# Performance work log

Measured on AMD Instinct MI355X. Metric: run time of the kernel, lower is better.

The kernel has to match this reference:

```python
import jax, jax.numpy as jnp
import numpy as np

NBINS = (128, 64, 32)
N_POINTS = 250_000
N_GENES = 5000
N_GENES_OI = 500
SUM_H = sum(NBINS)            # 224
SUM_W = sum(n - 1 for n in NBINS)  # 221


def _calculate_widths(unnormalized_widths):
    return jax.nn.softmax(unnormalized_widths, axis=-1)


def _calculate_bin_locations(widths):
    bl = jnp.cumsum(widths, axis=-1)
    bl = bl.at[..., -1].set(1.0)
    pad = [(0, 0)] * (bl.ndim - 1) + [(1, 0)]
    return jnp.pad(bl, pad)


def _calculate_heights(unnormalized_heights, widths):
    e = jnp.exp(unnormalized_heights)
    # trapezoid-rule area so pdf integrates to 1
    area = jnp.sum(0.5 * (e[..., :-1] + e[..., 1:]) * widths, axis=-1, keepdims=True)
    return e / area


def _calculate_bin_left_cdf(heights, widths):
    cdf = jnp.cumsum(0.5 * (heights[..., :-1] + heights[..., 1:]) * widths, axis=-1)
    cdf = cdf.at[..., -1].set(1.0)
    pad = [(0, 0)] * (cdf.ndim - 1) + [(1, 0)]
    return jnp.pad(cdf, pad)


def _quadratic_spline(x, widths, heights, bin_left_cdf, bin_locations):
    # all per-point: widths [N,nb], heights [N,nb+1], cdf/locations [N,nb+1]
    nb = widths.shape[-1]
    bin_idx = jnp.clip(jnp.sum(x[:, None] >= bin_locations, axis=-1) - 1, 0, nb - 1)

    def take(a, i):
        return jnp.take_along_axis(a, i[:, None], axis=-1)[:, 0]

    in_bl = take(bin_locations, bin_idx)
    in_cdf = take(bin_left_cdf, bin_idx)
    h_left = take(heights, bin_idx)
    h_right = take(heights, bin_idx + 1)
    w = take(widths, bin_idx)

    a = 0.5 * (h_right - h_left) * w
    b = h_left * w
    alpha = (x - in_bl) / w
    out = a * alpha * alpha + b * alpha + in_cdf
    logabsdet = jnp.log(alpha * (h_right - h_left) + h_left)
    return jnp.clip(out, 0.0, 1.0), logabsdet


def setup_inputs() -> dict:
    key = jax.random.key(0)
    k1, k2, k3, k4, k5, k6 = jax.random.split(key, 6)
    return {
        "x": jax.random.uniform(k1, (N_POINTS,), dtype=jnp.float32),
        "delta": jax.random.normal(k2, (N_POINTS, SUM_H), dtype=jnp.float32),
        "heights_weight": jax.random.normal(k3, (N_GENES, SUM_H), dtype=jnp.float32),
        "widths_weight": jax.random.normal(k4, (N_GENES, SUM_W), dtype=jnp.float32),
        "genes_oi": jax.random.randint(k5, (N_GENES_OI,), 0, N_GENES, dtype=jnp.int32),
        "local_gene_ix": jax.random.randint(k6, (N_POINTS,), 0, N_GENES_OI, dtype=jnp.int32),
    }


def reference(x, delta, heights_weight, widths_weight, genes_oi, local_gene_ix):
    # sparse embedding gather for the genes in the minibatch
    uh_all = heights_weight[genes_oi]   # [G_oi, sum_h]
    uw_all = widths_weight[genes_oi]    # [G_oi, sum_w]

    outputs = x
    logabsdet = jnp.zeros_like(x)
    h_off = 0
    w_off = 0
    d_off = 0
    for n in NBINS:
        uw = uw_all[:, w_off:w_off + (n - 1)]          # [G_oi, n-1]
        uh = uh_all[:, h_off:h_off + n]                # [G_oi, n]
        dh = delta[:, d_off:d_off + n]                 # [N, n]

        widths_g = _calculate_widths(uw)               # [G_oi, n-1]
        bin_loc_g = _calculate_bin_locations(widths_g) # [G_oi, n]

        widths = widths_g[local_gene_ix]               # [N, n-1]
        bin_locations = bin_loc_g[local_gene_ix]       # [N, n]
        uh_p = uh[local_gene_ix] + dh                  # [N, n]
        heights = _calculate_heights(uh_p, widths)     # [N, n]
        bin_left_cdf = _calculate_bin_left_cdf(heights, widths)  # [N, n]

        outputs, lad = _quadratic_spline(outputs, widths, heights, bin_left_cdf, bin_locations)
        logabsdet = logabsdet + lad

        h_off += n
        w_off += n - 1
        d_off += n
    return outputs, logabsdet
```

## Files before the change

kernel.cpp:

```cpp
#include <hip/hip_runtime.h>
#include <math.h>

#define SUM_H 224
#define SUM_W 221
#define ROWP  224

__global__ __launch_bounds__(64) void gene_tables_kernel(
    const float* __restrict__ widths_weight,
    const int*   __restrict__ genes_oi,
    float* __restrict__ bl_t,
    int n_genes)
{
    int g = blockIdx.x;
    if (g >= n_genes) return;
    int gi = genes_oi[g];
    int l  = threadIdx.x;

    const float* wsrc  = widths_weight + (size_t)gi * SUM_W;
    float*       bldst = bl_t + (size_t)g * ROWP;

    const int ns[3]   = {128, 64, 32};
    const int woff[3] = {0, 127, 190};
    const int toff[3] = {0, 128, 192};

    for (int lev = 0; lev < 3; lev++) {
        int m  = ns[lev] - 1;
        int j0 = 2 * l, j1 = 2 * l + 1;
        float u0 = (j0 < m) ? wsrc[woff[lev] + j0] : -1e30f;
        float u1 = (j1 < m) ? wsrc[woff[lev] + j1] : -1e30f;
        float mx = fmaxf(u0, u1);
        #pragma unroll
        for (int msk = 32; msk >= 1; msk >>= 1)
            mx = fmaxf(mx, __shfl_xor(mx, msk, 64));
        float e0 = (j0 < m) ? __expf(u0 - mx) : 0.f;
        float e1 = (j1 < m) ? __expf(u1 - mx) : 0.f;
        float local = e0 + e1;
        float incl  = local;
        #pragma unroll
        for (int off = 1; off < 64; off <<= 1) {
            float t = __shfl_up(incl, off, 64);
            if (l >= off) incl += t;
        }
        float total = __shfl(incl, 63, 64);
        float inv   = 1.0f / total;
        float excl  = incl - local;
        float c0 = (excl + e0) * inv;
        float c1 = (excl + e0 + e1) * inv;
        if (j0 <= m - 2) bldst[toff[lev] + j0 + 1] = c0;
        if (j1 <= m - 2) bldst[toff[lev] + j1 + 1] = c1;
        if (l == 0) {
            bldst[toff[lev]]     = 0.0f;
            bldst[toff[lev] + m] = 1.0f;
        }
    }
}

template<int CTRL>
__device__ __forceinline__ float dppf(float v) {
    return __builtin_bit_cast(float,
        __builtin_amdgcn_update_dpp(0, __builtin_bit_cast(int, v), CTRL, 0xF, 0xF, true));
}
template<int CTRL>
__device__ __forceinline__ int dppi(int v) {
    return __builtin_amdgcn_update_dpp(0, v, CTRL, 0xF, 0xF, true);
}
__device__ __forceinline__ float row16_sum(float v) {
    v += dppf<0x121>(v);
    v += dppf<0x122>(v);
    v += dppf<0x124>(v);
    v += dppf<0x128>(v);
    return v;
}
__device__ __forceinline__ int row16_sum_i(int v) {
    v += dppi<0x121>(v);
    v += dppi<0x122>(v);
    v += dppi<0x124>(v);
    v += dppi<0x128>(v);
    return v;
}

template<int K>
struct Lvl {
    float E[K + 1];
    float bl[K];
    float wh[K];
    float s[K];
    float bln;
    float inva;
    float larea;
};

template<int K>
__device__ __forceinline__ void lvl_fetch(const float* __restrict__ dh,
                                          const float* __restrict__ uh,
                                          const float* __restrict__ blp,
                                          int e, Lvl<K>& L)
{
    const int j = K * e;
    if constexpr (K == 8) {
        *(float4*)&L.E[0]  = *(const float4*)(uh  + j);
        *(float4*)&L.E[4]  = *(const float4*)(uh  + j + 4);
        *(float4*)&L.s[0]  = *(const float4*)(dh  + j);
        *(float4*)&L.s[4]  = *(const float4*)(dh  + j + 4);
        *(float4*)&L.bl[0] = *(const float4*)(blp + j);
        *(float4*)&L.bl[4] = *(const float4*)(blp + j + 4);
    } else if constexpr (K == 4) {
        *(float4*)&L.E[0]  = *(const float4*)(uh  + j);
        *(float4*)&L.s[0]  = *(const float4*)(dh  + j);
        *(float4*)&L.bl[0] = *(const float4*)(blp + j);
    } else {
        *(float2*)&L.E[0]  = *(const float2*)(uh  + j);
        *(float2*)&L.s[0]  = *(const float2*)(dh  + j);
        *(float2*)&L.bl[0] = *(const float2*)(blp + j);
    }
}

template<int K>
__device__ __forceinline__ void lvl_finish(int e, Lvl<K>& L)
{
    L.bln = __shfl_down(L.bl[0], 1, 16);
    #pragma unroll
    for (int k = 0; k < K; k++) L.E[k] = __expf(L.E[k] + L.s[k]);
    L.E[K] = __shfl_down(L.E[0], 1, 16);
    #pragma unroll
    for (int k = 0; k < K - 1; k++) L.wh[k] = 0.5f * (L.bl[k + 1] - L.bl[k]);
    L.wh[K - 1] = 0.5f * (L.bln - L.bl[K - 1]);
    #pragma unroll
    for (int k = 0; k < K; k++) L.s[k] = (L.E[k] + L.E[k + 1]) * L.wh[k];
    if (e == 15) L.s[K - 1] = 0.f;
    float a = 0.f;
    #pragma unroll
    for (int k = 0; k < K; k++) a += L.s[k];
    a = row16_sum(a);
    L.inva  = __builtin_amdgcn_rcpf(a);
    L.larea = __logf(a);
}

template<int N, int K>
__device__ __forceinline__ void lvl_apply(const Lvl<K>& L, float& x, float& lad)
{
    constexpr int LOGK = (K == 8) ? 3 : (K == 4) ? 2 : 1;
    int   cnt  = 0;
    float part = 0.f;
    #pragma unroll
    for (int k = 0; k < K; k++) cnt += (x >= L.bl[k]) ? 1 : 0;
    #pragma unroll
    for (int k = 0; k < K - 1; k++) part += (x >= L.bl[k + 1]) ? L.s[k] : 0.f;
    part += (x >= L.bln) ? L.s[K - 1] : 0.f;

    cnt  = row16_sum_i(cnt);
    part = row16_sum(part);

    int idx = cnt - 1;
    if (idx > N - 2) idx = N - 2;
    const int owner = idx >> LOGK;
    const int slot  = idx & (K - 1);

    float sE = L.E[0], sE1 = L.E[1], sB = L.bl[0], sW = L.wh[0];
    #pragma unroll
    for (int jj = 1; jj < K; jj++) {
        bool m = (slot == jj);
        sE  = m ? L.E[jj]     : sE;
        sE1 = m ? L.E[jj + 1] : sE1;
        sB  = m ? L.bl[jj]    : sB;
        sW  = m ? L.wh[jj]    : sW;
    }
    float El  = __shfl(sE,  owner, 16);
    float Er  = __shfl(sE1, owner, 16);
    float inb = __shfl(sB,  owner, 16);
    float whs = __shfl(sW,  owner, 16);

    float dE    = Er - El;
    float alpha = (x - inb) * __builtin_amdgcn_rcpf(whs + whs);
    float poly  = fmaf(fmaf(whs * dE, alpha, (El + El) * whs), alpha, part);
    float outv  = poly * L.inva;
    lad += __logf(fmaf(alpha, dE, El)) - L.larea;
    x = __builtin_amdgcn_fmed3f(outv, 0.0f, 1.0f);
}

__global__ __launch_bounds__(256) void spline_kernel(
    const float* __restrict__ x_in,
    const float* __restrict__ delta,
    const int*   __restrict__ lgx,
    const int*   __restrict__ genes_oi,
    const float* __restrict__ heights_weight,
    const float* __restrict__ bl_t,
    float* __restrict__ out,
    float* __restrict__ lad_out,
    int n_points)
{
    int tid = blockIdx.x * blockDim.x + threadIdx.x;
    int p = tid >> 4;
    int e = tid & 15;
    if (p >= n_points) return;

    int g  = lgx[p];
    int gi = genes_oi[g];
    const float* dh = delta          + (size_t)p  * SUM_H;
    const float* uh = heights_weight + (size_t)gi * SUM_H;
    const float* bl = bl_t + (size_t)g * ROWP;

    Lvl<8> L0; Lvl<4> L1; Lvl<2> L2;
    lvl_fetch<8>(dh,       uh,       bl,       e, L0);
    lvl_fetch<4>(dh + 128, uh + 128, bl + 128, e, L1);
    float x   = x_in[p];
    float lad = 0.f;
    lvl_finish<8>(e, L0);
    lvl_fetch<2>(dh + 192, uh + 192, bl + 192, e, L2);
    lvl_finish<4>(e, L1);
    lvl_apply<128, 8>(L0, x, lad);
    lvl_finish<2>(e, L2);
    lvl_apply<64,  4>(L1, x, lad);
    lvl_apply<32,  2>(L2, x, lad);

    if (e == 0) {
        out[p]     = x;
        lad_out[p] = lad;
    }
}

extern "C" void kernel_launch(void* const* d_in, const int* in_sizes, int n_in,
                              void* d_out, int out_size, void* d_ws, size_t ws_size,
                              hipStream_t stream)
{
    const float* x        = (const float*)d_in[0];
    const float* delta    = (const float*)d_in[1];
    const float* hw       = (const float*)d_in[2];
    const float* ww       = (const float*)d_in[3];
    const int*   genes_oi = (const int*)  d_in[4];
    const int*   lgx      = (const int*)  d_in[5];

    int n_points   = in_sizes[0];
    int n_genes_oi = in_sizes[4];

    float* bl_t = (float*)d_ws;

    hipLaunchKernelGGL(gene_tables_kernel, dim3(n_genes_oi), dim3(64), 0, stream,
                       ww, genes_oi, bl_t, n_genes_oi);

    const int threads = 256;
    const int ppb     = threads / 16;
    const int blocks  = (n_points + ppb - 1) / ppb;
    hipLaunchKernelGGL(spline_kernel, dim3(blocks), dim3(threads), 0, stream,
                       x, delta, lgx, genes_oi, hw, bl_t,
                       (float*)d_out, (float*)d_out + n_points, n_points);
}
```

Baseline: 328.4 us.

## Split spline kernel into level-0 pass and levels-1/2 pass with nontemporal loads

The fused spline kernel is split into two launches: one handles the 128-bin level and writes intermediate x and logabsdet to workspace, and the second handles the 64- and 32-bin levels. The aim is to cut per-thread register pressure so more waves can be resident, and to load the streamed delta rows with nontemporal hints so they do not pollute cache. The cost is an extra launch, an extra round-trip of intermediates through memory, and re-reading lgx/genes_oi in the second pass.

```diff
diff --git a/kernel.cpp b/kernel.cpp
--- a/kernel.cpp
+++ b/kernel.cpp
@@ -4,6 +4,16 @@
 #define SUM_H 224
 #define SUM_W 221
 #define ROWP  224
+
+typedef float f32x4 __attribute__((ext_vector_type(4)));
+typedef float f32x2 __attribute__((ext_vector_type(2)));
+
+__device__ __forceinline__ f32x4 ldnt4(const float* p) {
+    return __builtin_nontemporal_load((const f32x4*)p);
+}
+__device__ __forceinline__ f32x2 ldnt2(const float* p) {
+    return __builtin_nontemporal_load((const f32x2*)p);
+}
 
 __global__ __launch_bounds__(64) void gene_tables_kernel(
     const float* __restrict__ widths_weight,
@@ -65,17 +75,11 @@
     return __builtin_amdgcn_update_dpp(0, v, CTRL, 0xF, 0xF, true);
 }
 __device__ __forceinline__ float row16_sum(float v) {
-    v += dppf<0x121>(v);
-    v += dppf<0x122>(v);
-    v += dppf<0x124>(v);
-    v += dppf<0x128>(v);
+    v += dppf<0x121>(v); v += dppf<0x122>(v); v += dppf<0x124>(v); v += dppf<0x128>(v);
     return v;
 }
 __device__ __forceinline__ int row16_sum_i(int v) {
-    v += dppi<0x121>(v);
-    v += dppi<0x122>(v);
-    v += dppi<0x124>(v);
-    v += dppi<0x128>(v);
+    v += dppi<0x121>(v); v += dppi<0x122>(v); v += dppi<0x124>(v); v += dppi<0x128>(v);
     return v;
 }
 
@@ -98,20 +102,24 @@
 {
     const int j = K * e;
     if constexpr (K == 8) {
+        f32x4 d0 = ldnt4(dh + j), d1 = ldnt4(dh + j + 4);
         *(float4*)&L.E[0]  = *(const float4*)(uh  + j);
         *(float4*)&L.E[4]  = *(const float4*)(uh  + j + 4);
-        *(float4*)&L.s[0]  = *(const float4*)(dh  + j);
-        *(float4*)&L.s[4]  = *(const float4*)(dh  + j + 4);
         *(float4*)&L.bl[0] = *(const float4*)(blp + j);
         *(float4*)&L.bl[4] = *(const float4*)(blp + j + 4);
+        #pragma unroll
+        for (int k = 0; k < 4; k++) { L.s[k] = d0[k]; L.s[4 + k] = d1[k]; }
     } else if constexpr (K == 4) {
+        f32x4 d0 = ldnt4(dh + j);
         *(float4*)&L.E[0]  = *(const float4*)(uh  + j);
-        *(float4*)&L.s[0]  = *(const float4*)(dh  + j);
         *(float4*)&L.bl[0] = *(const float4*)(blp + j);
+        #pragma unroll
+        for (int k = 0; k < 4; k++) L.s[k] = d0[k];
     } else {
+        f32x2 d0 = ldnt2(dh + j);
         *(float2*)&L.E[0]  = *(const float2*)(uh  + j);
-        *(float2*)&L.s[0]  = *(const float2*)(dh  + j);
         *(float2*)&L.bl[0] = *(const float2*)(blp + j);
+        L.s[0] = d0[0]; L.s[1] = d0[1];
     }
 }
 
@@ -140,13 +148,18 @@
 __device__ __forceinline__ void lvl_apply(const Lvl<K>& L, float& x, float& lad)
 {
     constexpr int LOGK = (K == 8) ? 3 : (K == 4) ? 2 : 1;
+    bool c[K];
+    #pragma unroll
+    for (int k = 0; k < K; k++) c[k] = (x >= L.bl[k]);
+    bool cn = (x >= L.bln);
+
     int   cnt  = 0;
     float part = 0.f;
     #pragma unroll
-    for (int k = 0; k < K; k++) cnt += (x >= L.bl[k]) ? 1 : 0;
-    #pragma unroll
-    for (int k = 0; k < K - 1; k++) part += (x >= L.bl[k + 1]) ? L.s[k] : 0.f;
-    part += (x >= L.bln) ? L.s[K - 1] : 0.f;
+    for (int k = 0; k < K; k++) cnt += c[k] ? 1 : 0;
+    #pragma unroll
+    for (int k = 0; k < K - 1; k++) part += c[k + 1] ? L.s[k] : 0.f;
+    part += cn ? L.s[K - 1] : 0.f;
 
     cnt  = row16_sum_i(cnt);
     part = row16_sum(part);
@@ -178,8 +191,41 @@
     x = __builtin_amdgcn_fmed3f(outv, 0.0f, 1.0f);
 }
 
-__global__ __launch_bounds__(256) void spline_kernel(
+__global__ __launch_bounds__(256) void spline_pass0(
     const float* __restrict__ x_in,
+    const float* __restrict__ delta,
+    const int*   __restrict__ lgx,
+    const int*   __restrict__ genes_oi,
+    const float* __restrict__ heights_weight,
+    const float* __restrict__ bl_t,
+    float* __restrict__ x_mid,
+    float* __restrict__ lad_mid,
+    int n_points)
+{
+    int tid = blockIdx.x * blockDim.x + threadIdx.x;
+    int p = tid >> 4;
+    int e = tid & 15;
+    if (p >= n_points) return;
+
+    int g  = lgx[p];
+    int gi = genes_oi[g];
+    const float* dh = delta          + (size_t)p  * SUM_H;
+    const float* uh = heights_weight + (size_t)gi * SUM_H;
+    const float* bl = bl_t + (size_t)g * ROWP;
+
+    Lvl<8> L0;
+    lvl_fetch<8>(dh, uh, bl, e, L0);
+    float x = x_in[p];
+    float lad = 0.f;
+    lvl_finish<8>(e, L0);
+    lvl_apply<128, 8>(L0, x, lad);
+
+    if (e == 0) { x_mid[p] = x; lad_mid[p] = lad; }
+}
+
+__global__ __launch_bounds__(256) void spline_pass12(
+    const float* __restrict__ x_mid,
+    const float* __restrict__ lad_mid,
     const float* __restrict__ delta,
     const int*   __restrict__ lgx,
     const int*   __restrict__ genes_oi,
@@ -200,23 +246,17 @@
     const float* uh = heights_weight + (size_t)gi * SUM_H;
     const float* bl = bl_t + (size_t)g * ROWP;
 
-    Lvl<8> L0; Lvl<4> L1; Lvl<2> L2;
-    lvl_fetch<8>(dh,       uh,       bl,       e, L0);
+    Lvl<4> L1; Lvl<2> L2;
     lvl_fetch<4>(dh + 128, uh + 128, bl + 128, e, L1);
-    float x   = x_in[p];
-    float lad = 0.f;
-    lvl_finish<8>(e, L0);
     lvl_fetch<2>(dh + 192, uh + 192, bl + 192, e, L2);
+    float x   = x_mid[p];
+    float lad = lad_mid[p];
     lvl_finish<4>(e, L1);
-    lvl_apply<128, 8>(L0, x, lad);
     lvl_finish<2>(e, L2);
-    lvl_apply<64,  4>(L1, x, lad);
-    lvl_apply<32,  2>(L2, x, lad);
-
-    if (e == 0) {
-        out[p]     = x;
-        lad_out[p] = lad;
-    }
+    lvl_apply<64, 4>(L1, x, lad);
+    lvl_apply<32, 2>(L2, x, lad);
+
+    if (e == 0) { out[p] = x; lad_out[p] = lad; }
 }
 
 extern "C" void kernel_launch(void* const* d_in, const int* in_sizes, int n_in,
@@ -234,6 +274,10 @@
     int n_genes_oi = in_sizes[4];
 
     float* bl_t = (float*)d_ws;
+    size_t off  = (((size_t)n_genes_oi * ROWP) + 63) & ~(size_t)63;
+    float* x_mid   = bl_t + off;
+    size_t npad    = ((size_t)n_points + 63) & ~(size_t)63;
+    float* lad_mid = x_mid + npad;
 
     hipLaunchKernelGGL(gene_tables_kernel, dim3(n_genes_oi), dim3(64), 0, stream,
                        ww, genes_oi, bl_t, n_genes_oi);
@@ -241,7 +285,9 @@
     const int threads = 256;
     const int ppb     = threads / 16;
     const int blocks  = (n_points + ppb - 1) / ppb;
-    hipLaunchKernelGGL(spline_kernel, dim3(blocks), dim3(threads), 0, stream,
-                       x, delta, lgx, genes_oi, hw, bl_t,
+    hipLaunchKernelGGL(spline_pass0, dim3(blocks), dim3(threads), 0, stream,
+                       x, delta, lgx, genes_oi, hw, bl_t, x_mid, lad_mid, n_points);
+    hipLaunchKernelGGL(spline_pass12, dim3(blocks), dim3(threads), 0, stream,
+                       x_mid, lad_mid, delta, lgx, genes_oi, hw, bl_t,
                        (float*)d_out, (float*)d_out + n_points, n_points);
 }
```

Measured after the change: 336.7 us. +2.5%, slower.

## Precompute per-gene height-width products and fold log-det into a single log

Applied to the files above, without the earlier changes.

The per-gene table kernel now also exponentiates the gene height weights and stores the products 0.5*w*exp(h) for each bin edge, so the point kernel only exponentiates delta and combines it with table entries by FMAs. It drops the genes_oi indirection and the heights_weight reads from the point kernel. The three per-level log calls are replaced by one log of a running product plus a constant. Delta is read with nontemporal loads. The gene table triples in size, and taking one log of a product risks float underflow or overflow compared with summing logs.

```diff
diff --git a/kernel.cpp b/kernel.cpp
--- a/kernel.cpp
+++ b/kernel.cpp
@@ -3,12 +3,33 @@
 
 #define SUM_H 224
 #define SUM_W 221
-#define ROWP  224
+#define TROW  672
+
+#define OBL0 0
+#define OA0  128
+#define OB0  256
+#define OBL1 384
+#define OA1  448
+#define OB1  512
+#define OBL2 576
+#define OA2  608
+#define OB2  640
+
+typedef float f32x4 __attribute__((ext_vector_type(4)));
+typedef float f32x2 __attribute__((ext_vector_type(2)));
+
+__device__ __forceinline__ f32x4 ldnt4(const float* p) {
+    return __builtin_nontemporal_load((const f32x4*)p);
+}
+__device__ __forceinline__ f32x2 ldnt2(const float* p) {
+    return __builtin_nontemporal_load((const f32x2*)p);
+}
 
 __global__ __launch_bounds__(64) void gene_tables_kernel(
+    const float* __restrict__ heights_weight,
     const float* __restrict__ widths_weight,
     const int*   __restrict__ genes_oi,
-    float* __restrict__ bl_t,
+    float* __restrict__ tbl,
     int n_genes)
 {
     int g = blockIdx.x;
@@ -16,12 +37,16 @@
     int gi = genes_oi[g];
     int l  = threadIdx.x;
 
-    const float* wsrc  = widths_weight + (size_t)gi * SUM_W;
-    float*       bldst = bl_t + (size_t)g * ROWP;
+    const float* wsrc = widths_weight  + (size_t)gi * SUM_W;
+    const float* hsrc = heights_weight + (size_t)gi * SUM_H;
+    float*       row  = tbl + (size_t)g * TROW;
 
     const int ns[3]   = {128, 64, 32};
     const int woff[3] = {0, 127, 190};
-    const int toff[3] = {0, 128, 192};
+    const int hoff[3] = {0, 128, 192};
+    const int obl[3]  = {OBL0, OBL1, OBL2};
+    const int oa[3]   = {OA0, OA1, OA2};
+    const int ob[3]   = {OB0, OB1, OB2};
 
     for (int lev = 0; lev < 3; lev++) {
         int m  = ns[lev] - 1;
@@ -43,14 +68,23 @@
         }
         float total = __shfl(incl, 63, 64);
         float inv   = 1.0f / total;
+        float w0    = e0 * inv;
+        float w1    = e1 * inv;
         float excl  = incl - local;
         float c0 = (excl + e0) * inv;
         float c1 = (excl + e0 + e1) * inv;
-        if (j0 <= m - 2) bldst[toff[lev] + j0 + 1] = c0;
-        if (j1 <= m - 2) bldst[toff[lev] + j1 + 1] = c1;
+        if (j0 <= m - 2) row[obl[lev] + j0 + 1] = c0;
+        if (j1 <= m - 2) row[obl[lev] + j1 + 1] = c1;
+        float h0 = (j0 < m) ? __expf(hsrc[hoff[lev] + j0])     : 0.f;
+        float h1 = (j0 < m) ? __expf(hsrc[hoff[lev] + j0 + 1]) : 0.f;
+        float h2 = (j1 < m) ? __expf(hsrc[hoff[lev] + j1 + 1]) : 0.f;
+        if (j0 < m) { row[oa[lev] + j0] = 0.5f * w0 * h0;  row[ob[lev] + j0] = 0.5f * w0 * h1; }
+        if (j1 < m) { row[oa[lev] + j1] = 0.5f * w1 * h1;  row[ob[lev] + j1] = 0.5f * w1 * h2; }
         if (l == 0) {
-            bldst[toff[lev]]     = 0.0f;
-            bldst[toff[lev] + m] = 1.0f;
+            row[obl[lev]]     = 0.0f;
+            row[obl[lev] + m] = 1.0f;
+            row[oa[lev]  + m] = 0.0f;
+            row[ob[lev]  + m] = 0.0f;
         }
     }
 }
@@ -65,88 +99,60 @@
     return __builtin_amdgcn_update_dpp(0, v, CTRL, 0xF, 0xF, true);
 }
 __device__ __forceinline__ float row16_sum(float v) {
-    v += dppf<0x121>(v);
-    v += dppf<0x122>(v);
-    v += dppf<0x124>(v);
-    v += dppf<0x128>(v);
+    v += dppf<0x121>(v); v += dppf<0x122>(v); v += dppf<0x124>(v); v += dppf<0x128>(v);
     return v;
 }
 __device__ __forceinline__ int row16_sum_i(int v) {
-    v += dppi<0x121>(v);
-    v += dppi<0x122>(v);
-    v += dppi<0x124>(v);
-    v += dppi<0x128>(v);
+    v += dppi<0x121>(v); v += dppi<0x122>(v); v += dppi<0x124>(v); v += dppi<0x128>(v);
     return v;
 }
 
 template<int K>
 struct Lvl {
-    float E[K + 1];
     float bl[K];
-    float wh[K];
-    float s[K];
+    float a[K];
+    float b[K];
+    float d[K];
     float bln;
     float inva;
-    float larea;
 };
-
-template<int K>
-__device__ __forceinline__ void lvl_fetch(const float* __restrict__ dh,
-                                          const float* __restrict__ uh,
-                                          const float* __restrict__ blp,
-                                          int e, Lvl<K>& L)
-{
-    const int j = K * e;
-    if constexpr (K == 8) {
-        *(float4*)&L.E[0]  = *(const float4*)(uh  + j);
-        *(float4*)&L.E[4]  = *(const float4*)(uh  + j + 4);
-        *(float4*)&L.s[0]  = *(const float4*)(dh  + j);
-        *(float4*)&L.s[4]  = *(const float4*)(dh  + j + 4);
-        *(float4*)&L.bl[0] = *(const float4*)(blp + j);
-        *(float4*)&L.bl[4] = *(const float4*)(blp + j + 4);
-    } else if constexpr (K == 4) {
-        *(float4*)&L.E[0]  = *(const float4*)(uh  + j);
-        *(float4*)&L.s[0]  = *(const float4*)(dh  + j);
-        *(float4*)&L.bl[0] = *(const float4*)(blp + j);
-    } else {
-        *(float2*)&L.E[0]  = *(const float2*)(uh  + j);
-        *(float2*)&L.s[0]  = *(const float2*)(dh  + j);
-        *(float2*)&L.bl[0] = *(const float2*)(blp + j);
-    }
-}
 
 template<int K>
 __device__ __forceinline__ void lvl_finish(int e, Lvl<K>& L)
 {
-    L.bln = __shfl_down(L.bl[0], 1, 16);
-    #pragma unroll
-    for (int k = 0; k < K; k++) L.E[k] = __expf(L.E[k] + L.s[k]);
-    L.E[K] = __shfl_down(L.E[0], 1, 16);
-    #pragma unroll
-    for (int k = 0; k < K - 1; k++) L.wh[k] = 0.5f * (L.bl[k + 1] - L.bl[k]);
-    L.wh[K - 1] = 0.5f * (L.bln - L.bl[K - 1]);
-    #pragma unroll
-    for (int k = 0; k < K; k++) L.s[k] = (L.E[k] + L.E[k + 1]) * L.wh[k];
-    if (e == 15) L.s[K - 1] = 0.f;
-    float a = 0.f;
-    #pragma unroll
-    for (int k = 0; k < K; k++) a += L.s[k];
-    a = row16_sum(a);
-    L.inva  = __builtin_amdgcn_rcpf(a);
-    L.larea = __logf(a);
+    float ed[K];
+    #pragma unroll
+    for (int k = 0; k < K; k++) ed[k] = __expf(L.d[k]);
+    float edn = __shfl_down(ed[0], 1, 16);
+    L.bln     = __shfl_down(L.bl[0], 1, 16);
+    #pragma unroll
+    for (int k = 0; k < K; k++) L.a[k] *= ed[k];
+    #pragma unroll
+    for (int k = 0; k < K - 1; k++) L.b[k] = fmaf(L.b[k], ed[k + 1], L.a[k]);
+    L.b[K - 1] = fmaf(L.b[K - 1], edn, L.a[K - 1]);
+    float lane = 0.f;
+    #pragma unroll
+    for (int k = 0; k < K; k++) lane += L.b[k];
+    L.inva = __builtin_amdgcn_rcpf(row16_sum(lane));
 }
 
 template<int N, int K>
-__device__ __forceinline__ void lvl_apply(const Lvl<K>& L, float& x, float& lad)
+__device__ __forceinline__ void lvl_apply(int e, const Lvl<K>& L, float& x, float& prod)
 {
     constexpr int LOGK = (K == 8) ? 3 : (K == 4) ? 2 : 1;
+    bool c[K];
+    #pragma unroll
+    for (int k = 0; k < K; k++) c[k] = (x >= L.bl[k]);
+    bool not15 = (e != 15);
+    bool cn = not15 && (x >= L.bln);
+
     int   cnt  = 0;
     float part = 0.f;
     #pragma unroll
-    for (int k = 0; k < K; k++) cnt += (x >= L.bl[k]) ? 1 : 0;
-    #pragma unroll
-    for (int k = 0; k < K - 1; k++) part += (x >= L.bl[k + 1]) ? L.s[k] : 0.f;
-    part += (x >= L.bln) ? L.s[K - 1] : 0.f;
+    for (int k = 0; k < K; k++) cnt += c[k] ? 1 : 0;
+    #pragma unroll
+    for (int k = 0; k < K - 1; k++) part += c[k + 1] ? L.b[k] : 0.f;
+    part += cn ? L.b[K - 1] : 0.f;
 
     cnt  = row16_sum_i(cnt);
     part = row16_sum(part);
@@ -154,37 +160,37 @@
     int idx = cnt - 1;
     if (idx > N - 2) idx = N - 2;
     const int owner = idx >> LOGK;
-    const int slot  = idx & (K - 1);
-
-    float sE = L.E[0], sE1 = L.E[1], sB = L.bl[0], sW = L.wh[0];
+
+    float sB = L.bl[0], sB1 = L.bl[1], sP = L.a[0], sS = L.b[0];
     #pragma unroll
     for (int jj = 1; jj < K; jj++) {
-        bool m = (slot == jj);
-        sE  = m ? L.E[jj]     : sE;
-        sE1 = m ? L.E[jj + 1] : sE1;
-        sB  = m ? L.bl[jj]    : sB;
-        sW  = m ? L.wh[jj]    : sW;
-    }
-    float El  = __shfl(sE,  owner, 16);
-    float Er  = __shfl(sE1, owner, 16);
-    float inb = __shfl(sB,  owner, 16);
-    float whs = __shfl(sW,  owner, 16);
-
-    float dE    = Er - El;
-    float alpha = (x - inb) * __builtin_amdgcn_rcpf(whs + whs);
-    float poly  = fmaf(fmaf(whs * dE, alpha, (El + El) * whs), alpha, part);
-    float outv  = poly * L.inva;
-    lad += __logf(fmaf(alpha, dE, El)) - L.larea;
-    x = __builtin_amdgcn_fmed3f(outv, 0.0f, 1.0f);
+        bool  m   = (jj == K - 1) ? (c[jj] && not15) : c[jj];
+        float nb1 = (jj == K - 1) ? L.bln : L.bl[jj + 1];
+        sB  = m ? L.bl[jj] : sB;
+        sB1 = m ? nb1      : sB1;
+        sP  = m ? L.a[jj]  : sP;
+        sS  = m ? L.b[jj]  : sS;
+    }
+    float sw = sB1 - sB;
+
+    float inb = __shfl(sB, owner, 16);
+    float ww  = __shfl(sw, owner, 16);
+    float P   = __shfl(sP, owner, 16);
+    float S   = __shfl(sS, owner, 16);
+
+    float dEh   = fmaf(-2.f, P, S);
+    float rw    = __builtin_amdgcn_rcpf(ww);
+    float alpha = (x - inb) * rw;
+    float poly  = fmaf(fmaf(dEh, alpha, P + P), alpha, part);
+    x = __builtin_amdgcn_fmed3f(poly * L.inva, 0.0f, 1.0f);
+    prod *= fmaf(alpha, dEh, P) * (rw * L.inva);
 }
 
 __global__ __launch_bounds__(256) void spline_kernel(
     const float* __restrict__ x_in,
     const float* __restrict__ delta,
     const int*   __restrict__ lgx,
-    const int*   __restrict__ genes_oi,
-    const float* __restrict__ heights_weight,
-    const float* __restrict__ bl_t,
+    const float* __restrict__ tbl,
     float* __restrict__ out,
     float* __restrict__ lad_out,
     int n_points)
@@ -194,28 +200,54 @@
     int e = tid & 15;
     if (p >= n_points) return;
 
-    int g  = lgx[p];
-    int gi = genes_oi[g];
-    const float* dh = delta          + (size_t)p  * SUM_H;
-    const float* uh = heights_weight + (size_t)gi * SUM_H;
-    const float* bl = bl_t + (size_t)g * ROWP;
+    const float* dh = delta + (size_t)p * SUM_H;
 
     Lvl<8> L0; Lvl<4> L1; Lvl<2> L2;
-    lvl_fetch<8>(dh,       uh,       bl,       e, L0);
-    lvl_fetch<4>(dh + 128, uh + 128, bl + 128, e, L1);
-    float x   = x_in[p];
-    float lad = 0.f;
+    {
+        const int j = 8 * e;
+        f32x4 d0 = ldnt4(dh + j), d1 = ldnt4(dh + j + 4);
+        #pragma unroll
+        for (int k = 0; k < 4; k++) { L0.d[k] = d0[k]; L0.d[4 + k] = d1[k]; }
+        f32x4 d2 = ldnt4(dh + 128 + 4 * e);
+        #pragma unroll
+        for (int k = 0; k < 4; k++) L1.d[k] = d2[k];
+        f32x2 d3 = ldnt2(dh + 192 + 2 * e);
+        L2.d[0] = d3[0]; L2.d[1] = d3[1];
+    }
+    float x = x_in[p];
+    int   g = lgx[p];
+    const float* row = tbl + (size_t)g * TROW;
+
+    {
+        const int j = 8 * e;
+        *(float4*)&L0.bl[0] = *(const float4*)(row + OBL0 + j);
+        *(float4*)&L0.bl[4] = *(const float4*)(row + OBL0 + j + 4);
+        *(float4*)&L0.a[0]  = *(const float4*)(row + OA0  + j);
+        *(float4*)&L0.a[4]  = *(const float4*)(row + OA0  + j + 4);
+        *(float4*)&L0.b[0]  = *(const float4*)(row + OB0  + j);
+        *(float4*)&L0.b[4]  = *(const float4*)(row + OB0  + j + 4);
+        const int j1 = 4 * e;
+        *(float4*)&L1.bl[0] = *(const float4*)(row + OBL1 + j1);
+        *(float4*)&L1.a[0]  = *(const float4*)(row + OA1  + j1);
+        *(float4*)&L1.b[0]  = *(const float4*)(row + OB1  + j1);
+        const int j2 = 2 * e;
+        *(float2*)&L2.bl[0] = *(const float2*)(row + OBL2 + j2);
+        *(float2*)&L2.a[0]  = *(const float2*)(row + OA2  + j2);
+        *(float2*)&L2.b[0]  = *(const float2*)(row + OB2  + j2);
+    }
+
     lvl_finish<8>(e, L0);
-    lvl_fetch<2>(dh + 192, uh + 192, bl + 192, e, L2);
     lvl_finish<4>(e, L1);
-    lvl_apply<128, 8>(L0, x, lad);
     lvl_finish<2>(e, L2);
-    lvl_apply<64,  4>(L1, x, lad);
-    lvl_apply<32,  2>(L2, x, lad);
+
+    float prod = 1.f;
+    lvl_apply<128, 8>(e, L0, x, prod);
+    lvl_apply<64,  4>(e, L1, x, prod);
+    lvl_apply<32,  2>(e, L2, x, prod);
 
     if (e == 0) {
         out[p]     = x;
-        lad_out[p] = lad;
+        lad_out[p] = __logf(prod) + 2.0794415416798357f;
     }
 }
 
@@ -233,15 +265,15 @@
     int n_points   = in_sizes[0];
     int n_genes_oi = in_sizes[4];
 
-    float* bl_t = (float*)d_ws;
+    float* tbl = (float*)d_ws;
 
     hipLaunchKernelGGL(gene_tables_kernel, dim3(n_genes_oi), dim3(64), 0, stream,
-                       ww, genes_oi, bl_t, n_genes_oi);
+                       hw, ww, genes_oi, tbl, n_genes_oi);
 
     const int threads = 256;
     const int ppb     = threads / 16;
     const int blocks  = (n_points + ppb - 1) / ppb;
     hipLaunchKernelGGL(spline_kernel, dim3(blocks), dim3(threads), 0, stream,
-                       x, delta, lgx, genes_oi, hw, bl_t,
+                       x, delta, lgx, tbl,
                        (float*)d_out, (float*)d_out + n_points, n_points);
 }
```

New measurement: 338.4 us. 3.0% more time.
